# Kernel optimization log

Hardware: AMD Instinct MI355X
Metric: run time of the kernel (lower is better)

The kernel has to match this reference:

```python
import jax, jax.numpy as jnp
import numpy as np

B, M, K = 8, 4096, 16
C = 64       # input_dim
D = 64       # d_model


def _lin(key, fan_in, fan_out):
    k1, k2 = jax.random.split(key)
    bound = 1.0 / np.sqrt(fan_in)
    W = jax.random.uniform(k1, (fan_out, fan_in), minval=-bound, maxval=bound, dtype=jnp.float32)
    b = jax.random.uniform(k2, (fan_out,), minval=-bound, maxval=bound, dtype=jnp.float32)
    return W, b


def setup_inputs() -> dict:
    key = jax.random.key(0)
    ks = jax.random.split(key, 12)
    x = jax.random.normal(ks[0], (B, M, K, C), dtype=jnp.float32)
    xyz = jax.random.normal(ks[1], (B, M, K, 3), dtype=jnp.float32)
    Wq, bq = _lin(ks[2], C, D)
    Wk, bk = _lin(ks[3], C, D)
    Wv, bv = _lin(ks[4], C, D)
    Wp1, bp1 = _lin(ks[5], 3, D)
    Wp2, bp2 = _lin(ks[6], D, D)
    Wa1, ba1 = _lin(ks[7], D, D)
    Wa2, ba2 = _lin(ks[8], D, D)
    W2, b2 = _lin(ks[9], D, C)
    return dict(x=x, xyz=xyz, Wq=Wq, bq=bq, Wk=Wk, bk=bk, Wv=Wv, bv=bv,
                Wp1=Wp1, bp1=bp1, Wp2=Wp2, bp2=bp2,
                Wa1=Wa1, ba1=ba1, Wa2=Wa2, ba2=ba2, W2=W2, b2=b2)


def reference(x, xyz, Wq, bq, Wk, bk, Wv, bv, Wp1, bp1, Wp2, bp2,
              Wa1, ba1, Wa2, ba2, W2, b2):
    lin = lambda t, W, b: jnp.matmul(t, W.T) + b
    raw_feature = x[:, :, 0, :]                 # [B,M,C]
    raw_xyz = xyz[:, :, 0:1, :]                 # [B,M,1,3]
    q = lin(raw_feature, Wq, bq)                # [B,M,D]
    k = lin(x, Wk, bk)                          # [B,M,K,D]
    v = lin(x, Wv, bv)                          # [B,M,K,D]
    rel = xyz - raw_xyz                         # [B,M,K,3]
    pos_enc = lin(jax.nn.relu(lin(rel, Wp1, bp1)), Wp2, bp2)  # [B,M,K,D]
    h = q[:, :, None, :] - k + pos_enc          # [B,M,K,D]
    attn_logits = lin(jax.nn.relu(lin(h, Wa1, ba1)), Wa2, ba2)
    attn = jax.nn.softmax(attn_logits / np.sqrt(D), axis=-2)  # softmax over K
    res = jnp.einsum('bmnf,bmnf->bmf', attn, v + pos_enc)
    return lin(res, W2, b2) + raw_feature       # [B,M,C]
```

## Files before the change

kernel.cpp:

```cpp
#include <hip/hip_runtime.h>

#define NM 4096
#define NK 16
#define NC 64

typedef __attribute__((ext_vector_type(8))) short s8v;
typedef __attribute__((ext_vector_type(4))) float f4v;
typedef __attribute__((ext_vector_type(2))) unsigned int u2v;

__device__ __forceinline__ short f2bf(float f) {
  return __builtin_bit_cast(short, (__bf16)f);
}
__device__ __forceinline__ float bf2f(unsigned short s) {
  return __builtin_bit_cast(float, ((unsigned)s) << 16);
}
__device__ __forceinline__ unsigned pk2(float a, float b) {
  unsigned short lo = __builtin_bit_cast(unsigned short, (__bf16)a);
  unsigned short hi = __builtin_bit_cast(unsigned short, (__bf16)b);
  return (unsigned)lo | ((unsigned)hi << 16);
}
__device__ __forceinline__ s8v pack8(f4v a, f4v b) {
  s8v r;
  r[0]=f2bf(a[0]); r[1]=f2bf(a[1]); r[2]=f2bf(a[2]); r[3]=f2bf(a[3]);
  r[4]=f2bf(b[0]); r[5]=f2bf(b[1]); r[6]=f2bf(b[2]); r[7]=f2bf(b[3]);
  return r;
}

#define MFMA(a,b,c) __builtin_amdgcn_mfma_f32_16x16x32_bf16((a),(b),(c),0,0,0)

#define HSTRIDE 72
#define TB (16*HSTRIDE)

__global__ void precomp_kernel(const float* __restrict__ Wq, const float* __restrict__ bq,
                               const float* __restrict__ Wk, const float* __restrict__ bk,
                               const float* __restrict__ Wp2,const float* __restrict__ bp2,
                               const float* __restrict__ Wa1,const float* __restrict__ ba1,
                               float* __restrict__ ws) {
  const int gid = blockIdx.x * 256 + threadIdx.x;
  if (gid < 3*4096) {
    const int m = gid >> 12, e = gid & 4095, i = e >> 6, j = e & 63;
    const float* R = Wa1 + i*64;
    float s = 0.f;
    if (m == 0)      { for (int l = 0; l < 64; ++l) s += R[l] * Wq [l*64 + j]; }
    else if (m == 1) { for (int l = 0; l < 64; ++l) s -= R[l] * Wk [l*64 + j]; }
    else             { for (int l = 0; l < 64; ++l) s += R[l] * Wp2[l*64 + j]; }
    ws[gid] = s;
  } else if (gid < 3*4096 + 64) {
    const int i = gid - 3*4096;
    const float* R = Wa1 + i*64;
    float s = 0.f;
    for (int l = 0; l < 64; ++l) s += R[l] * bq[l];
    ws[gid] = s;
  } else if (gid < 3*4096 + 128) {
    const int i = gid - (3*4096 + 64);
    const float* R = Wa1 + i*64;
    float s = ba1[i];
    for (int l = 0; l < 64; ++l) s += R[l] * (bp2[l] - bk[l]);
    ws[gid] = s;
  }
}

__global__ __attribute__((amdgpu_flat_work_group_size(256, 256)))
           __attribute__((amdgpu_waves_per_eu(1, 8)))
void lattn_kernel(const float* __restrict__ x,  const float* __restrict__ xyz,
                  const float* __restrict__ Wp1,const float* __restrict__ bp1,
                  const float* __restrict__ Wp2,const float* __restrict__ bp2,
                  const float* __restrict__ Wv, const float* __restrict__ bv,
                  const float* __restrict__ Wa2,const float* __restrict__ ba2,
                  const float* __restrict__ W2, const float* __restrict__ b2,
                  const float* __restrict__ ws,
                  float* __restrict__ out) {
  __shared__ __align__(16) short wlds[5*8*64*8];
  __shared__ __align__(16) short qres[4*TB];

  const int tid = threadIdx.x;
  const float* wak = ws + 4096;
  const float* wap = ws + 8192;
  const float* bqa = ws + 12288;
  const float* bcv = ws + 12352;

  for (int idx = tid; idx < 5*8*64; idx += 256) {
    const int mat = idx >> 9;
    const int rem = idx & 511;
    const int f   = rem >> 6;
    const int ln  = rem & 63;
    const int t = f >> 1, h = f & 1;
    const int cc = ln & 15, qq = ln >> 4;
    const int n = 16*t + cc;
    const float* W = (mat==0) ? wak : (mat==1) ? Wv : (mat==2) ? Wp2 : (mat==3) ? wap : Wa2;
    s8v v;
    #pragma unroll
    for (int j = 0; j < 8; ++j) {
      const int kp = h*32 + qq*8 + j;
      int k;
      if (mat == 4)      k = 16*(2*h + (j>>2)) + 4*qq + (j&3);
      else if (mat >= 2) k = ((kp & 3) << 4) | (kp >> 2);
      else               k = kp;
      v[j] = f2bf(W[n*64 + k]);
    }
    *(s8v*)&wlds[(size_t)idx * 8] = v;
  }
  __syncthreads();

  const int w    = tid >> 6;
  const int lane = tid & 63;
  const int c    = lane & 15;
  const int lq   = lane >> 4;

  const int gw  = blockIdx.x * 4 + w;
  const int gp0 = gw << 4;
  const int b   = gp0 >> 12;
  const int m0  = gp0 & (NM - 1);

  short* qbuf = qres + w * TB;

  f4v wp1v[16];
  #pragma unroll
  for (int i = 0; i < 16; ++i) {
    const int jj = i & 7, h = i >> 3;
    const int n = 16*(jj&3) + 2*lq + (jj>>2) + 8*h;
    f4v t4;
    t4[0] = Wp1[n*3+0]; t4[1] = Wp1[n*3+1]; t4[2] = Wp1[n*3+2]; t4[3] = bp1[n];
    wp1v[i] = t4;
  }
  float bvpe[4], ba2f[4], bcf[4];
  #pragma unroll
  for (int t = 0; t < 4; ++t) {
    const int n = 16*t + c;
    bvpe[t] = bv[n] + bp2[n];
    ba2f[t] = ba2[n]; bcf[t] = bcv[n];
  }

  const long ptbase = (long)(b * NM + m0);

  {
    const float* xr = x + (ptbase + c) * (long)(NK*NC) + 8*lq;
    s8v rA0 = pack8(*(const f4v*)xr,        *(const f4v*)(xr+4));
    s8v rA1 = pack8(*(const f4v*)(xr+32),   *(const f4v*)(xr+36));
    #pragma unroll
    for (int t = 0; t < 4; ++t) {
      const float* wr = ws + (16*t + c)*64 + 8*lq;
      s8v w0 = pack8(*(const f4v*)wr,       *(const f4v*)(wr+4));
      s8v w1 = pack8(*(const f4v*)(wr+32),  *(const f4v*)(wr+36));
      const float bb = bqa[16*t + c];
      f4v acc = {bb, bb, bb, bb};
      acc = MFMA(rA0, w0, acc);
      acc = MFMA(rA1, w1, acc);
      #pragma unroll
      for (int r = 0; r < 4; ++r)
        qbuf[(4*lq + r)*HSTRIDE + 16*t + c] = f2bf(acc[r] + bcf[t]);
    }
  }

  f4v nxr0, nxr1, nxr2, nxr3;
  float nza[3], nzb[3];
  {
    const float* xr = x + ptbase * (long)(NK*NC) + c*NC + 8*lq;
    nxr0 = *(const f4v*)xr;      nxr1 = *(const f4v*)(xr+4);
    nxr2 = *(const f4v*)(xr+32); nxr3 = *(const f4v*)(xr+36);
    const float* zp = xyz + ptbase * (long)(NK*3);
    nza[0] = zp[c*3+0]; nza[1] = zp[c*3+1]; nza[2] = zp[c*3+2];
    nzb[0] = zp[0];     nzb[1] = zp[1];     nzb[2] = zp[2];
  }

  #pragma unroll 1
  for (int p = 0; p < 16; ++p) {
    s8v xA0 = pack8(nxr0, nxr1);
    s8v xA1 = pack8(nxr2, nxr3);
    const float rx = nza[0] - nzb[0];
    const float ry = nza[1] - nzb[1];
    const float rz = nza[2] - nzb[2];
    if (p < 15) {
      const long prow = ptbase + p + 1;
      const float* xr = x + prow * (long)(NK*NC) + c*NC + 8*lq;
      nxr0 = *(const f4v*)xr;      nxr1 = *(const f4v*)(xr+4);
      nxr2 = *(const f4v*)(xr+32); nxr3 = *(const f4v*)(xr+36);
      const float* zp = xyz + prow * (long)(NK*3);
      nza[0] = zp[c*3+0]; nza[1] = zp[c*3+1]; nza[2] = zp[c*3+2];
      nzb[0] = zp[0];     nzb[1] = zp[1];     nzb[2] = zp[2];
    }

    f4v base[4];
    #pragma unroll
    for (int t = 0; t < 4; ++t) {
      u2v q2 = *(const u2v*)&qbuf[p*HSTRIDE + 16*t + 4*lq];
      base[t][0] = __builtin_bit_cast(float, q2[0] << 16);
      base[t][1] = __builtin_bit_cast(float, q2[0] & 0xffff0000u);
      base[t][2] = __builtin_bit_cast(float, q2[1] << 16);
      base[t][3] = __builtin_bit_cast(float, q2[1] & 0xffff0000u);
    }

    s8v pA0, pA1;
    #pragma unroll
    for (int i = 0; i < 8; ++i) {
      f4v w0v = wp1v[i], w1v = wp1v[8+i];
      float v0 = fmaxf(fmaf(w0v[0], rx, fmaf(w0v[1], ry, fmaf(w0v[2], rz, w0v[3]))), 0.0f);
      float v1 = fmaxf(fmaf(w1v[0], rx, fmaf(w1v[1], ry, fmaf(w1v[2], rz, w1v[3]))), 0.0f);
      pA0[i] = f2bf(v0);
      pA1[i] = f2bf(v1);
    }

    f4v s[4];
    #pragma unroll
    for (int t = 0; t < 4; ++t) {
      const short* wb = &wlds[(0*512 + 2*t*64 + lane) * 8];
      f4v acc = MFMA(*(const s8v*)wb,         xA0, base[t]);
      acc     = MFMA(*(const s8v*)(wb + 512), xA1, acc);
      s[t] = acc;
    }
    #pragma unroll
    for (int t = 0; t < 4; ++t) {
      const short* wb = &wlds[(3*512 + 2*t*64 + lane) * 8];
      f4v acc = MFMA(*(const s8v*)wb,         pA0, s[t]);
      acc     = MFMA(*(const s8v*)(wb + 512), pA1, acc);
      #pragma unroll
      for (int r = 0; r < 4; ++r) s[t][r] = fmaxf(acc[r], 0.0f);
    }
    s8v aA0 = pack8(s[0], s[1]);
    s8v aA1 = pack8(s[2], s[3]);

    f4v lg[4];
    #pragma unroll
    for (int t = 0; t < 4; ++t) {
      const short* wb = &wlds[(4*512 + 2*t*64 + lane) * 8];
      f4v acc = {ba2f[t], ba2f[t], ba2f[t], ba2f[t]};
      acc = MFMA(aA0, *(const s8v*)wb,         acc);
      acc = MFMA(aA1, *(const s8v*)(wb + 512), acc);
      lg[t] = acc;
    }

    f4v vpe[4];
    #pragma unroll
    for (int t = 0; t < 4; ++t) {
      const short* wb1 = &wlds[(1*512 + 2*t*64 + lane) * 8];
      const short* wb2 = &wlds[(2*512 + 2*t*64 + lane) * 8];
      f4v acc = {bvpe[t], bvpe[t], bvpe[t], bvpe[t]};
      acc = MFMA(xA0, *(const s8v*)wb1, acc);
      acc = MFMA(xA1, *(const s8v*)(wb1 + 512), acc);
      acc = MFMA(pA0, *(const s8v*)wb2, acc);
      acc = MFMA(pA1, *(const s8v*)(wb2 + 512), acc);
      vpe[t] = acc;
    }

    #pragma unroll
    for (int t = 0; t < 4; ++t) {
      f4v l = lg[t];
      f4v e;
      #pragma unroll
      for (int r = 0; r < 4; ++r) e[r] = exp2f(l[r] * 0.18033688011112043f);
      float sm = (e[0] + e[1]) + (e[2] + e[3]);
      sm += __shfl_xor(sm, 16);
      sm += __shfl_xor(sm, 32);
      float pr = 0.0f;
      #pragma unroll
      for (int r = 0; r < 4; ++r) pr += e[r] * vpe[t][r];
      pr += __shfl_xor(pr, 16);
      pr += __shfl_xor(pr, 32);
      pr *= 1.0f / sm;
      if (lq == 0) qbuf[p*HSTRIDE + 16*t + c] = f2bf(pr);
    }
  }

  {
    s8v resA0 = *(const s8v*)&qbuf[c*HSTRIDE + 8*lq];
    s8v resA1 = *(const s8v*)&qbuf[c*HSTRIDE + 32 + 8*lq];
    #pragma unroll
    for (int t = 0; t < 4; ++t) {
      const float* wr = W2 + (16*t + c)*64 + 8*lq;
      s8v w0 = pack8(*(const f4v*)wr,      *(const f4v*)(wr+4));
      s8v w1 = pack8(*(const f4v*)(wr+32), *(const f4v*)(wr+36));
      const float bb = b2[16*t + c];
      f4v acc = {bb, bb, bb, bb};
      acc = MFMA(resA0, w0, acc);
      acc = MFMA(resA1, w1, acc);
      #pragma unroll
      for (int r = 0; r < 4; ++r) {
        const long pr2 = ptbase + 4*lq + r;
        out[pr2*NC + 16*t + c] = acc[r] + x[pr2*(long)(NK*NC) + 16*t + c];
      }
    }
  }
}

extern "C" void kernel_launch(void* const* d_in, const int* in_sizes, int n_in,
                              void* d_out, int out_size, void* d_ws, size_t ws_size,
                              hipStream_t stream) {
  (void)in_sizes; (void)n_in; (void)out_size; (void)ws_size;
  const float* x   = (const float*)d_in[0];
  const float* xyz = (const float*)d_in[1];
  const float* Wq  = (const float*)d_in[2];
  const float* bq  = (const float*)d_in[3];
  const float* Wk  = (const float*)d_in[4];
  const float* bk  = (const float*)d_in[5];
  const float* Wv  = (const float*)d_in[6];
  const float* bv  = (const float*)d_in[7];
  const float* Wp1 = (const float*)d_in[8];
  const float* bp1 = (const float*)d_in[9];
  const float* Wp2 = (const float*)d_in[10];
  const float* bp2 = (const float*)d_in[11];
  const float* Wa1 = (const float*)d_in[12];
  const float* ba1 = (const float*)d_in[13];
  const float* Wa2 = (const float*)d_in[14];
  const float* ba2 = (const float*)d_in[15];
  const float* W2  = (const float*)d_in[16];
  const float* b2  = (const float*)d_in[17];
  float* out = (float*)d_out;
  float* ws  = (float*)d_ws;

  precomp_kernel<<<dim3(49), dim3(256), 0, stream>>>(Wq, bq, Wk, bk, Wp2, bp2, Wa1, ba1, ws);
  lattn_kernel<<<dim3(512), dim3(256), 0, stream>>>(
      x, xyz, Wp1, bp1, Wp2, bp2, Wv, bv, Wa2, ba2, W2, b2, ws, out);
}
```

Baseline: 267.6 us.

## Halve points per wave, pre-pack bf16 weights in a separate precompute kernel

```diff
diff --git a/kernel.cpp b/kernel.cpp
--- a/kernel.cpp
+++ b/kernel.cpp
@@ -13,11 +13,6 @@
 }
 __device__ __forceinline__ float bf2f(unsigned short s) {
   return __builtin_bit_cast(float, ((unsigned)s) << 16);
-}
-__device__ __forceinline__ unsigned pk2(float a, float b) {
-  unsigned short lo = __builtin_bit_cast(unsigned short, (__bf16)a);
-  unsigned short hi = __builtin_bit_cast(unsigned short, (__bf16)b);
-  return (unsigned)lo | ((unsigned)hi << 16);
 }
 __device__ __forceinline__ s8v pack8(f4v a, f4v b) {
   s8v r;
@@ -29,7 +24,7 @@
 #define MFMA(a,b,c) __builtin_amdgcn_mfma_f32_16x16x32_bf16((a),(b),(c),0,0,0)
 
 #define HSTRIDE 72
-#define TB (16*HSTRIDE)
+#define TB8 (8*HSTRIDE)
 
 __global__ void precomp_kernel(const float* __restrict__ Wq, const float* __restrict__ bq,
                                const float* __restrict__ Wk, const float* __restrict__ bk,
@@ -60,8 +55,42 @@
   }
 }
 
+__global__ void precomp2_kernel(const float* __restrict__ Wv,
+                                const float* __restrict__ Wp2,
+                                const float* __restrict__ Wa2,
+                                const float* __restrict__ W2,
+                                float* __restrict__ ws) {
+  const int g = blockIdx.x * 256 + threadIdx.x;
+  if (g >= 7*512) return;
+  const int mat = g >> 9, rem = g & 511;
+  const int f = rem >> 6, ln = rem & 63;
+  const int t = f >> 1, h = f & 1;
+  const int cc = ln & 15, qq = ln >> 4;
+  const int n = 16*t + cc;
+  const float* W =
+    (mat==0) ? ws + 4096 :
+    (mat==1) ? Wv :
+    (mat==2) ? Wp2 :
+    (mat==3) ? ws + 8192 :
+    (mat==4) ? Wa2 :
+    (mat==5) ? ws :
+               W2;
+  short* dst = (short*)(ws + 12544) + (size_t)g * 8;
+  s8v v;
+  #pragma unroll
+  for (int j = 0; j < 8; ++j) {
+    const int kp = h*32 + qq*8 + j;
+    int k;
+    if (mat == 4)                  k = 16*(2*h + (j>>2)) + 4*qq + (j&3);
+    else if (mat == 2 || mat == 3) k = ((kp & 3) << 4) | (kp >> 2);
+    else                           k = kp;
+    v[j] = f2bf(W[n*64 + k]);
+  }
+  *(s8v*)dst = v;
+}
+
 __global__ __attribute__((amdgpu_flat_work_group_size(256, 256)))
-           __attribute__((amdgpu_waves_per_eu(1, 8)))
+           __attribute__((amdgpu_waves_per_eu(3, 8)))
 void lattn_kernel(const float* __restrict__ x,  const float* __restrict__ xyz,
                   const float* __restrict__ Wp1,const float* __restrict__ bp1,
                   const float* __restrict__ Wp2,const float* __restrict__ bp2,
@@ -71,34 +100,26 @@
                   const float* __restrict__ ws,
                   float* __restrict__ out) {
   __shared__ __align__(16) short wlds[5*8*64*8];
-  __shared__ __align__(16) short qres[4*TB];
+  __shared__ __align__(16) short qres[4*TB8];
+  __shared__ __align__(16) f4v  wp1t[4*17];
 
   const int tid = threadIdx.x;
-  const float* wak = ws + 4096;
-  const float* wap = ws + 8192;
   const float* bqa = ws + 12288;
   const float* bcv = ws + 12352;
-
-  for (int idx = tid; idx < 5*8*64; idx += 256) {
-    const int mat = idx >> 9;
-    const int rem = idx & 511;
-    const int f   = rem >> 6;
-    const int ln  = rem & 63;
-    const int t = f >> 1, h = f & 1;
-    const int cc = ln & 15, qq = ln >> 4;
-    const int n = 16*t + cc;
-    const float* W = (mat==0) ? wak : (mat==1) ? Wv : (mat==2) ? Wp2 : (mat==3) ? wap : Wa2;
-    s8v v;
-    #pragma unroll
-    for (int j = 0; j < 8; ++j) {
-      const int kp = h*32 + qq*8 + j;
-      int k;
-      if (mat == 4)      k = 16*(2*h + (j>>2)) + 4*qq + (j&3);
-      else if (mat >= 2) k = ((kp & 3) << 4) | (kp >> 2);
-      else               k = kp;
-      v[j] = f2bf(W[n*64 + k]);
-    }
-    *(s8v*)&wlds[(size_t)idx * 8] = v;
+  const short* wsb = (const short*)(ws + 12544);
+
+  #pragma unroll
+  for (int i = 0; i < 10; ++i) {
+    const int g = tid + i*256;
+    *(s8v*)&wlds[(size_t)g*8] = *(const s8v*)&wsb[(size_t)g*8];
+  }
+  if (tid < 64) {
+    const int lqv = tid >> 4, ii = tid & 15;
+    const int jj = ii & 7, h = ii >> 3;
+    const int n = 16*(jj&3) + 2*lqv + (jj>>2) + 8*h;
+    f4v t4;
+    t4[0] = Wp1[n*3+0]; t4[1] = Wp1[n*3+1]; t4[2] = Wp1[n*3+2]; t4[3] = bp1[n];
+    wp1t[lqv*17 + ii] = t4;
   }
   __syncthreads();
 
@@ -108,21 +129,12 @@
   const int lq   = lane >> 4;
 
   const int gw  = blockIdx.x * 4 + w;
-  const int gp0 = gw << 4;
+  const int gp0 = gw << 3;
   const int b   = gp0 >> 12;
   const int m0  = gp0 & (NM - 1);
 
-  short* qbuf = qres + w * TB;
-
-  f4v wp1v[16];
-  #pragma unroll
-  for (int i = 0; i < 16; ++i) {
-    const int jj = i & 7, h = i >> 3;
-    const int n = 16*(jj&3) + 2*lq + (jj>>2) + 8*h;
-    f4v t4;
-    t4[0] = Wp1[n*3+0]; t4[1] = Wp1[n*3+1]; t4[2] = Wp1[n*3+2]; t4[3] = bp1[n];
-    wp1v[i] = t4;
-  }
+  short* qbuf = qres + w * TB8;
+
   float bvpe[4], ba2f[4], bcf[4];
   #pragma unroll
   for (int t = 0; t < 4; ++t) {
@@ -134,21 +146,22 @@
   const long ptbase = (long)(b * NM + m0);
 
   {
-    const float* xr = x + (ptbase + c) * (long)(NK*NC) + 8*lq;
+    const float* xr = x + (ptbase + (c & 7)) * (long)(NK*NC) + 8*lq;
     s8v rA0 = pack8(*(const f4v*)xr,        *(const f4v*)(xr+4));
     s8v rA1 = pack8(*(const f4v*)(xr+32),   *(const f4v*)(xr+36));
     #pragma unroll
     for (int t = 0; t < 4; ++t) {
-      const float* wr = ws + (16*t + c)*64 + 8*lq;
-      s8v w0 = pack8(*(const f4v*)wr,       *(const f4v*)(wr+4));
-      s8v w1 = pack8(*(const f4v*)(wr+32),  *(const f4v*)(wr+36));
+      s8v w0 = *(const s8v*)&wsb[(size_t)(5*512 + 2*t*64 + lane)*8];
+      s8v w1 = *(const s8v*)&wsb[(size_t)(5*512 + (2*t+1)*64 + lane)*8];
       const float bb = bqa[16*t + c];
       f4v acc = {bb, bb, bb, bb};
       acc = MFMA(rA0, w0, acc);
       acc = MFMA(rA1, w1, acc);
-      #pragma unroll
-      for (int r = 0; r < 4; ++r)
-        qbuf[(4*lq + r)*HSTRIDE + 16*t + c] = f2bf(acc[r] + bcf[t]);
+      if (lq < 2) {
+        #pragma unroll
+        for (int r = 0; r < 4; ++r)
+          qbuf[(4*lq + r)*HSTRIDE + 16*t + c] = f2bf(acc[r] + bcf[t]);
+      }
     }
   }
 
@@ -164,13 +177,13 @@
   }
 
   #pragma unroll 1
-  for (int p = 0; p < 16; ++p) {
+  for (int p = 0; p < 8; ++p) {
     s8v xA0 = pack8(nxr0, nxr1);
     s8v xA1 = pack8(nxr2, nxr3);
     const float rx = nza[0] - nzb[0];
     const float ry = nza[1] - nzb[1];
     const float rz = nza[2] - nzb[2];
-    if (p < 15) {
+    if (p < 7) {
       const long prow = ptbase + p + 1;
       const float* xr = x + prow * (long)(NK*NC) + c*NC + 8*lq;
       nxr0 = *(const f4v*)xr;      nxr1 = *(const f4v*)(xr+4);
@@ -193,7 +206,8 @@
     s8v pA0, pA1;
     #pragma unroll
     for (int i = 0; i < 8; ++i) {
-      f4v w0v = wp1v[i], w1v = wp1v[8+i];
+      f4v w0v = wp1t[lq*17 + i];
+      f4v w1v = wp1t[lq*17 + 8 + i];
       float v0 = fmaxf(fmaf(w0v[0], rx, fmaf(w0v[1], ry, fmaf(w0v[2], rz, w0v[3]))), 0.0f);
       float v1 = fmaxf(fmaf(w1v[0], rx, fmaf(w1v[1], ry, fmaf(w1v[2], rz, w1v[3]))), 0.0f);
       pA0[i] = f2bf(v0);
@@ -262,21 +276,22 @@
   }
 
   {
-    s8v resA0 = *(const s8v*)&qbuf[c*HSTRIDE + 8*lq];
-    s8v resA1 = *(const s8v*)&qbuf[c*HSTRIDE + 32 + 8*lq];
-    #pragma unroll
-    for (int t = 0; t < 4; ++t) {
-      const float* wr = W2 + (16*t + c)*64 + 8*lq;
-      s8v w0 = pack8(*(const f4v*)wr,      *(const f4v*)(wr+4));
-      s8v w1 = pack8(*(const f4v*)(wr+32), *(const f4v*)(wr+36));
+    s8v resA0 = *(const s8v*)&qbuf[(c & 7)*HSTRIDE + 8*lq];
+    s8v resA1 = *(const s8v*)&qbuf[(c & 7)*HSTRIDE + 32 + 8*lq];
+    #pragma unroll
+    for (int t = 0; t < 4; ++t) {
+      s8v w0 = *(const s8v*)&wsb[(size_t)(6*512 + 2*t*64 + lane)*8];
+      s8v w1 = *(const s8v*)&wsb[(size_t)(6*512 + (2*t+1)*64 + lane)*8];
       const float bb = b2[16*t + c];
       f4v acc = {bb, bb, bb, bb};
       acc = MFMA(resA0, w0, acc);
       acc = MFMA(resA1, w1, acc);
-      #pragma unroll
-      for (int r = 0; r < 4; ++r) {
-        const long pr2 = ptbase + 4*lq + r;
-        out[pr2*NC + 16*t + c] = acc[r] + x[pr2*(long)(NK*NC) + 16*t + c];
+      if (lq < 2) {
+        #pragma unroll
+        for (int r = 0; r < 4; ++r) {
+          const long pr2 = ptbase + 4*lq + r;
+          out[pr2*NC + 16*t + c] = acc[r] + x[pr2*(long)(NK*NC) + 16*t + c];
+        }
       }
     }
   }
@@ -308,6 +323,7 @@
   float* ws  = (float*)d_ws;
 
   precomp_kernel<<<dim3(49), dim3(256), 0, stream>>>(Wq, bq, Wk, bk, Wp2, bp2, Wa1, ba1, ws);
-  lattn_kernel<<<dim3(512), dim3(256), 0, stream>>>(
+  precomp2_kernel<<<dim3(14), dim3(256), 0, stream>>>(Wv, Wp2, Wa2, W2, ws);
+  lattn_kernel<<<dim3(1024), dim3(256), 0, stream>>>(
       x, xyz, Wp1, bp1, Wp2, bp2, Wv, bv, Wa2, ba2, W2, b2, ws, out);
 }
```

Result: slower. 546.3 us (+104.1%).
